# Kernel optimization log

Hardware: AMD Instinct MI355X
Metric: run time of the kernel (lower is better)

Reference implementation:

```python
import math
import jax, jax.numpy as jnp
import numpy as np

D_MODEL = 1024
NUM_HEADS = 16
HEAD_DIM = D_MODEL // NUM_HEADS
CAUSAL = True


def setup_inputs() -> dict:
    key = jax.random.key(0)
    ks = jax.random.split(key, 9)
    B, S = 2, 2048
    s = 1.0 / math.sqrt(D_MODEL)
    x = jax.random.normal(ks[0], (B, S, D_MODEL), dtype=jnp.float32)
    Wq = jax.random.normal(ks[1], (D_MODEL, D_MODEL), dtype=jnp.float32) * s
    bq = jax.random.normal(ks[2], (D_MODEL,), dtype=jnp.float32) * 0.01
    Wk = jax.random.normal(ks[3], (D_MODEL, D_MODEL), dtype=jnp.float32) * s
    bk = jax.random.normal(ks[4], (D_MODEL,), dtype=jnp.float32) * 0.01
    Wv = jax.random.normal(ks[5], (D_MODEL, D_MODEL), dtype=jnp.float32) * s
    bv = jax.random.normal(ks[6], (D_MODEL,), dtype=jnp.float32) * 0.01
    Wo = jax.random.normal(ks[7], (D_MODEL, D_MODEL), dtype=jnp.float32) * s
    bo = jax.random.normal(ks[8], (D_MODEL,), dtype=jnp.float32) * 0.01
    return {"x": x, "Wq": Wq, "bq": bq, "Wk": Wk, "bk": bk,
            "Wv": Wv, "bv": bv, "Wo": Wo, "bo": bo}


def reference(x, Wq, bq, Wk, bk, Wv, bv, Wo, bo):
    B, S, _ = x.shape
    # projections (torch Linear: x @ W.T + b; here W already stored as [in,out])
    q = x @ Wq + bq
    k = x @ Wk + bk
    v = x @ Wv + bv
    # split heads -> [B, H, S, hd]
    def split(t):
        return t.reshape(B, S, NUM_HEADS, HEAD_DIM).transpose(0, 2, 1, 3)
    q, k, v = split(q), split(k), split(v)
    scores = jnp.einsum('bhqd,bhkd->bhqk', q, k) / math.sqrt(HEAD_DIM)
    if CAUSAL:
        causal = jnp.tril(jnp.ones((S, S), dtype=bool))  # True = keep
        scores = jnp.where(causal, scores, -jnp.inf)
    attn = jax.nn.softmax(scores, axis=-1)
    out = jnp.einsum('bhqk,bhkd->bhqd', attn, v)
    out = out.transpose(0, 2, 1, 3).reshape(B, S, D_MODEL)
    return out @ Wo + bo
```

## Files before the change

### kernel.cpp

```cpp
#include <hip/hip_runtime.h>
#include <hip/hip_bf16.h>

typedef __bf16 bf16_t;
typedef __bf16 v8bf __attribute__((ext_vector_type(8)));
typedef float  v4f  __attribute__((ext_vector_type(4)));

#define MFMA16(a, b, c) __builtin_amdgcn_mfma_f32_16x16x32_bf16((a), (b), (c), 0, 0, 0)

#define GLDS16(g, l) __builtin_amdgcn_global_load_lds(                         \
    (const __attribute__((address_space(1))) void*)(g),                        \
    (__attribute__((address_space(3))) void*)(l), 16, 0, 0)

#define VMEMCNT(n) asm volatile("s_waitcnt vmcnt(" #n ")" ::: "memory")
#define SBAR()     __builtin_amdgcn_s_barrier()
#define SFENCE()   __builtin_amdgcn_sched_barrier(0)

#define B_SZ   2
#define SEQ    2048
#define DM     1024
#define NH     16
#define HD     64
#define M_TOT  4096

#define QSCALE 0.18033688011112043f

__global__ __launch_bounds__(256)
void conv_x_kernel(const float* __restrict__ src, bf16_t* __restrict__ dst)
{
    int i = (blockIdx.x * 256 + threadIdx.x) * 8;
    float4 a = *reinterpret_cast<const float4*>(src + i);
    float4 b = *reinterpret_cast<const float4*>(src + i + 4);
    union { bf16_t h[8]; int4 v; } u;
    u.h[0] = (bf16_t)a.x; u.h[1] = (bf16_t)a.y; u.h[2] = (bf16_t)a.z; u.h[3] = (bf16_t)a.w;
    u.h[4] = (bf16_t)b.x; u.h[5] = (bf16_t)b.y; u.h[6] = (bf16_t)b.z; u.h[7] = (bf16_t)b.w;
    *reinterpret_cast<int4*>(dst + i) = u.v;
}

__global__ __launch_bounds__(256)
void conv_wt_kernel(const float* __restrict__ Wq, const float* __restrict__ Wk,
                    const float* __restrict__ Wv, const float* __restrict__ Wo,
                    bf16_t* __restrict__ WqkvT, bf16_t* __restrict__ WoT)
{
    __shared__ float t[32][33];
    const int z = blockIdx.z;
    const float* src = (z == 0) ? Wq : (z == 1) ? Wk : (z == 2) ? Wv : Wo;
    bf16_t* dst = (z < 3) ? (WqkvT + (size_t)z * 1048576) : WoT;
    const int tx = threadIdx.x & 31, ty = threadIdx.x >> 5;
    const int c0 = blockIdx.x * 32, r0 = blockIdx.y * 32;
#pragma unroll
    for (int i = 0; i < 4; ++i)
        t[ty + i * 8][tx] = src[(size_t)(r0 + ty + i * 8) * DM + c0 + tx];
    __syncthreads();
#pragma unroll
    for (int i = 0; i < 4; ++i)
        dst[(size_t)(c0 + ty + i * 8) * DM + r0 + tx] = (bf16_t)t[tx][ty + i * 8];
}

__global__ __launch_bounds__(256)
void gemm_qkv_kernel(const bf16_t* __restrict__ A, const bf16_t* __restrict__ BT,
                     const float* __restrict__ b0, const float* __restrict__ b1,
                     const float* __restrict__ b2,
                     bf16_t* __restrict__ oQ, bf16_t* __restrict__ oK,
                     bf16_t* __restrict__ oV)
{
    __shared__ __align__(16) bf16_t As[2 * 128 * 64];
    __shared__ __align__(16) bf16_t Bs[2 * 192 * 64];

    const int tid  = threadIdx.x;
    const int lane = tid & 63;
    const int wave = tid >> 6;
    const int wm   = (wave >> 1) * 64;
    const int wn   = (wave & 1) * 96;
    const int quad = lane >> 4;
    const int l15  = lane & 15;
    const int l7   = l15 & 7;

    const int n0 = blockIdx.x * 192;
    const int m0 = blockIdx.y * 128;

    const bf16_t *ap[4], *bp[6];
#pragma unroll
    for (int i = 0; i < 4; ++i) {
        int cidx = (wave * 4 + i) * 64 + lane;
        int r = cidx >> 3;
        int c = (cidx & 7) ^ (r & 7);
        ap[i] = A + (size_t)(m0 + r) * DM + c * 8;
    }
#pragma unroll
    for (int i = 0; i < 6; ++i) {
        int cidx = (wave * 6 + i) * 64 + lane;
        int r = cidx >> 3;
        int c = (cidx & 7) ^ (r & 7);
        bp[i] = BT + (size_t)(n0 + r) * DM + c * 8;
    }

    const v4f vzero = {0.f, 0.f, 0.f, 0.f};
    v4f acc[4][6];
#pragma unroll
    for (int mt = 0; mt < 4; ++mt)
#pragma unroll
        for (int nt = 0; nt < 6; ++nt) acc[mt][nt] = vzero;

#pragma unroll
    for (int i = 0; i < 4; ++i) { GLDS16(ap[i], As + (wave * 4 + i) * 512); ap[i] += 64; }
#pragma unroll
    for (int i = 0; i < 6; ++i) { GLDS16(bp[i], Bs + (wave * 6 + i) * 512); bp[i] += 64; }
#pragma unroll
    for (int i = 0; i < 4; ++i) { GLDS16(ap[i], As + 8192 + (wave * 4 + i) * 512); ap[i] += 64; }
#pragma unroll
    for (int i = 0; i < 6; ++i) { GLDS16(bp[i], Bs + 12288 + (wave * 6 + i) * 512); bp[i] += 64; }

    for (int it = 0; it < 16; ++it) {
        const int cur = it & 1;
        if (it < 15) { VMEMCNT(10); } else { VMEMCNT(0); }
        SBAR(); SFENCE();
#pragma unroll
        for (int ks = 0; ks < 2; ++ks) {
            v8bf af[4], bfq[6];
#pragma unroll
            for (int mt = 0; mt < 4; ++mt)
                af[mt] = *reinterpret_cast<const v8bf*>(
                    &As[cur * 8192 + (wm + mt * 16 + l15) * 64 + ((ks * 4 + quad) ^ l7) * 8]);
#pragma unroll
            for (int nt = 0; nt < 6; ++nt)
                bfq[nt] = *reinterpret_cast<const v8bf*>(
                    &Bs[cur * 12288 + (wn + nt * 16 + l15) * 64 + ((ks * 4 + quad) ^ l7) * 8]);
#pragma unroll
            for (int mt = 0; mt < 4; ++mt)
#pragma unroll
                for (int nt = 0; nt < 6; ++nt)
                    acc[mt][nt] = MFMA16(bfq[nt], af[mt], acc[mt][nt]);
        }
        SFENCE(); SBAR();
        if (it < 14) {
#pragma unroll
            for (int i = 0; i < 4; ++i) {
                GLDS16(ap[i], As + cur * 8192 + (wave * 4 + i) * 512);
                ap[i] += 64;
            }
#pragma unroll
            for (int i = 0; i < 6; ++i) {
                GLDS16(bp[i], Bs + cur * 12288 + (wave * 6 + i) * 512);
                bp[i] += 64;
            }
        }
    }

#pragma unroll
    for (int nt = 0; nt < 6; ++nt) {
        const int cf0 = n0 + wn + nt * 16;
        const int mat = cf0 >> 10;
        const int cw  = cf0 & 1023;
        if (mat != 2) {
            bf16_t* dst = (mat == 0) ? oQ : oK;
            const float scale = (mat == 0) ? QSCALE : 1.0f;
            const float* bias = (mat == 0) ? b0 : b1;
            const int h = cw >> 6;
            const int dbase = (cw & 63) + quad * 4;
            float4 bv = *reinterpret_cast<const float4*>(bias + cw + quad * 4);
#pragma unroll
            for (int mt = 0; mt < 4; ++mt) {
                int srow = m0 + wm + mt * 16 + l15;
                int b = srow >> 11, s = srow & 2047;
                union { bf16_t hh[4]; int2 v; } u;
                u.hh[0] = (bf16_t)((acc[mt][nt][0] + bv.x) * scale);
                u.hh[1] = (bf16_t)((acc[mt][nt][1] + bv.y) * scale);
                u.hh[2] = (bf16_t)((acc[mt][nt][2] + bv.z) * scale);
                u.hh[3] = (bf16_t)((acc[mt][nt][3] + bv.w) * scale);
                *reinterpret_cast<int2*>(
                    dst + ((size_t)(b * NH + h) * SEQ + s) * HD + dbase) = u.v;
            }
        } else {
#pragma unroll
            for (int r = 0; r < 4; ++r) {
                int cwe = cw + quad * 4 + r;
                float bvv = b2[cwe];
                int h = cwe >> 6, d = cwe & 63;
#pragma unroll
                for (int mt = 0; mt < 4; ++mt) {
                    int srow = m0 + wm + mt * 16 + l15;
                    int b = srow >> 11, s = srow & 2047;
                    oV[((size_t)(b * NH + h) * HD + d) * SEQ + s] =
                        (bf16_t)(acc[mt][nt][r] + bvv);
                }
            }
        }
    }
}

__global__ __launch_bounds__(256)
void gemm_o_kernel(const bf16_t* __restrict__ A, const bf16_t* __restrict__ BT,
                   const float* __restrict__ bias, float* __restrict__ out)
{
    __shared__ __align__(16) bf16_t As[2 * 128 * 64];
    __shared__ __align__(16) bf16_t Bs[2 * 64 * 64];

    const int tid  = threadIdx.x;
    const int lane = tid & 63;
    const int wave = tid >> 6;
    const int wm   = (wave >> 1) * 64;
    const int wn   = (wave & 1) * 32;
    const int quad = lane >> 4;
    const int l15  = lane & 15;
    const int l7   = l15 & 7;

    const int n0 = blockIdx.x * 64;
    const int m0 = blockIdx.y * 128;

    const bf16_t *ap[4], *bp[2];
#pragma unroll
    for (int i = 0; i < 4; ++i) {
        int cidx = (wave * 4 + i) * 64 + lane;
        int r = cidx >> 3;
        int c = (cidx & 7) ^ (r & 7);
        ap[i] = A + (size_t)(m0 + r) * DM + c * 8;
    }
#pragma unroll
    for (int i = 0; i < 2; ++i) {
        int cidx = (wave * 2 + i) * 64 + lane;
        int r = cidx >> 3;
        int c = (cidx & 7) ^ (r & 7);
        bp[i] = BT + (size_t)(n0 + r) * DM + c * 8;
    }

    const v4f vzero = {0.f, 0.f, 0.f, 0.f};
    v4f acc[4][2];
#pragma unroll
    for (int mt = 0; mt < 4; ++mt)
#pragma unroll
        for (int nt = 0; nt < 2; ++nt) acc[mt][nt] = vzero;

#pragma unroll
    for (int i = 0; i < 4; ++i) { GLDS16(ap[i], As + (wave * 4 + i) * 512); ap[i] += 64; }
#pragma unroll
    for (int i = 0; i < 2; ++i) { GLDS16(bp[i], Bs + (wave * 2 + i) * 512); bp[i] += 64; }
#pragma unroll
    for (int i = 0; i < 4; ++i) { GLDS16(ap[i], As + 8192 + (wave * 4 + i) * 512); ap[i] += 64; }
#pragma unroll
    for (int i = 0; i < 2; ++i) { GLDS16(bp[i], Bs + 4096 + (wave * 2 + i) * 512); bp[i] += 64; }

    for (int it = 0; it < 16; ++it) {
        const int cur = it & 1;
        if (it < 15) { VMEMCNT(6); } else { VMEMCNT(0); }
        SBAR(); SFENCE();
#pragma unroll
        for (int ks = 0; ks < 2; ++ks) {
            v8bf af[4], bfq[2];
#pragma unroll
            for (int mt = 0; mt < 4; ++mt)
                af[mt] = *reinterpret_cast<const v8bf*>(
                    &As[cur * 8192 + (wm + mt * 16 + l15) * 64 + ((ks * 4 + quad) ^ l7) * 8]);
#pragma unroll
            for (int nt = 0; nt < 2; ++nt)
                bfq[nt] = *reinterpret_cast<const v8bf*>(
                    &Bs[cur * 4096 + (wn + nt * 16 + l15) * 64 + ((ks * 4 + quad) ^ l7) * 8]);
#pragma unroll
            for (int mt = 0; mt < 4; ++mt)
#pragma unroll
                for (int nt = 0; nt < 2; ++nt)
                    acc[mt][nt] = MFMA16(af[mt], bfq[nt], acc[mt][nt]);
        }
        SFENCE(); SBAR();
        if (it < 14) {
#pragma unroll
            for (int i = 0; i < 4; ++i) {
                GLDS16(ap[i], As + cur * 8192 + (wave * 4 + i) * 512);
                ap[i] += 64;
            }
#pragma unroll
            for (int i = 0; i < 2; ++i) {
                GLDS16(bp[i], Bs + cur * 4096 + (wave * 2 + i) * 512);
                bp[i] += 64;
            }
        }
    }

#pragma unroll
    for (int mt = 0; mt < 4; ++mt) {
#pragma unroll
        for (int nt = 0; nt < 2; ++nt) {
            int col = n0 + wn + nt * 16 + l15;
            float bv = bias[col];
#pragma unroll
            for (int r = 0; r < 4; ++r) {
                int row = m0 + wm + mt * 16 + quad * 4 + r;
                out[(size_t)row * DM + col] = acc[mt][nt][r] + bv;
            }
        }
    }
}

__global__ __launch_bounds__(256)
void attn_kernel(const bf16_t* __restrict__ Q, const bf16_t* __restrict__ K,
                 const bf16_t* __restrict__ Vt, bf16_t* __restrict__ O)
{
    __shared__ __align__(16) bf16_t Ks[3][64 * 64];
    __shared__ __align__(16) bf16_t Vs[3][64 * 64];
    __shared__ __align__(16) bf16_t Ps[64 * 72];

    const int tid  = threadIdx.x;
    const int lane = tid & 63;
    const int w    = tid >> 6;
    const int quad = lane >> 4;
    const int l15  = lane & 15;
    const int l7   = lane & 7;

    const int bid = blockIdx.x;
    const int xcd = bid & 7;
    const int j   = bid >> 3;
    const int bh  = (xcd << 2) | (j >> 4);
    const int p   = j & 15;
    const size_t base = (size_t)bh * SEQ * HD;
    const bf16_t* Qg = Q  + base;
    const bf16_t* Kg = K  + base;
    const bf16_t* Vg = Vt + base;

    const int rr0 = tid >> 3;
    const int cc0 = (tid & 7) ^ (rr0 & 7);
    const int bO = bh >> 4, hO = bh & 15;
    const v4f vzero = {0.f, 0.f, 0.f, 0.f};

    for (int phase = 0; phase < 2; ++phase) {
        const int t  = phase ? (31 - p) : p;
        const int q0 = t * 64;
        const int qg = q0 + w * 16 + l15;

        v8bf qf[2];
        {
            const bf16_t* qrow = Qg + (size_t)qg * HD;
            qf[0] = *reinterpret_cast<const v8bf*>(qrow + quad * 8);
            qf[1] = *reinterpret_cast<const v8bf*>(qrow + 32 + quad * 8);
        }

        const bf16_t* kp0 = Kg + (size_t)rr0 * HD + cc0 * 8;
        const bf16_t* kp1 = kp0 + 32 * HD;
        const bf16_t* vp0 = Vg + (size_t)rr0 * SEQ + cc0 * 8;
        const bf16_t* vp1 = vp0 + (size_t)32 * SEQ;

        v4f acc_o[4];
#pragma unroll
        for (int dt = 0; dt < 4; ++dt) acc_o[dt] = vzero;
        float lrow = 0.f;

        VMEMCNT(0);
        SBAR();
        GLDS16(kp0, &Ks[0][w * 512]);
        GLDS16(kp1, &Ks[0][2048 + w * 512]);
        GLDS16(vp0, &Vs[0][w * 512]);
        GLDS16(vp1, &Vs[0][2048 + w * 512]);
        kp0 += 64 * HD;  kp1 += 64 * HD;  vp0 += 64;  vp1 += 64;
        if (t >= 1) {
            GLDS16(kp0, &Ks[1][w * 512]);
            GLDS16(kp1, &Ks[1][2048 + w * 512]);
            GLDS16(vp0, &Vs[1][w * 512]);
            GLDS16(vp1, &Vs[1][2048 + w * 512]);
            kp0 += 64 * HD;  kp1 += 64 * HD;  vp0 += 64;  vp1 += 64;
        }
        if (t >= 2) {
            GLDS16(kp0, &Ks[2][w * 512]);
            GLDS16(kp1, &Ks[2][2048 + w * 512]);
            GLDS16(vp0, &Vs[2][w * 512]);
            GLDS16(vp1, &Vs[2][2048 + w * 512]);
            kp0 += 64 * HD;  kp1 += 64 * HD;  vp0 += 64;  vp1 += 64;
        }

        int cur = 0;
        for (int kt = 0; kt <= t; ++kt) {
            if (kt + 2 <= t)      { VMEMCNT(8); }
            else if (kt + 1 <= t) { VMEMCNT(4); }
            else                  { VMEMCNT(0); }
            SBAR(); SFENCE();

            v4f st[4];
#pragma unroll
            for (int ktile = 0; ktile < 4; ++ktile) st[ktile] = vzero;
#pragma unroll
            for (int ks = 0; ks < 2; ++ks) {
                v8bf kb[4];
#pragma unroll
                for (int ktile = 0; ktile < 4; ++ktile)
                    kb[ktile] = *reinterpret_cast<const v8bf*>(
                        &Ks[cur][(ktile * 16 + l15) * 64 + ((ks * 4 + quad) ^ l7) * 8]);
#pragma unroll
                for (int ktile = 0; ktile < 4; ++ktile)
                    st[ktile] = MFMA16(kb[ktile], qf[ks], st[ktile]);
            }

            const bool diagI = (kt == t);
            float rs = 0.f;
            const int prow = (w * 16 + l15) * 72;
#pragma unroll
            for (int ktile = 0; ktile < 4; ++ktile) {
                union { bf16_t h[4]; int2 v; } u;
                if (diagI && ktile > w) {
                    u.v.x = 0; u.v.y = 0;
                } else if (diagI && ktile == w) {
#pragma unroll
                    for (int r = 0; r < 4; ++r) {
                        int kg = kt * 64 + ktile * 16 + quad * 4 + r;
                        float pv = (kg > qg) ? 0.f : __builtin_amdgcn_exp2f(st[ktile][r]);
                        rs += pv;
                        u.h[r] = (bf16_t)pv;
                    }
                } else {
#pragma unroll
                    for (int r = 0; r < 4; ++r) {
                        float pv = __builtin_amdgcn_exp2f(st[ktile][r]);
                        rs += pv;
                        u.h[r] = (bf16_t)pv;
                    }
                }
                *reinterpret_cast<int2*>(&Ps[prow + ktile * 16 + quad * 4]) = u.v;
            }
            rs += __shfl_xor(rs, 16);
            rs += __shfl_xor(rs, 32);
            lrow += rs;

#pragma unroll
            for (int ks = 0; ks < 2; ++ks) {
                v8bf vb[4];
#pragma unroll
                for (int dt = 0; dt < 4; ++dt)
                    vb[dt] = *reinterpret_cast<const v8bf*>(
                        &Vs[cur][(dt * 16 + l15) * 64 + ((ks * 4 + quad) ^ l7) * 8]);
                v8bf pf = *reinterpret_cast<const v8bf*>(
                    &Ps[(w * 16 + l15) * 72 + ks * 32 + quad * 8]);
#pragma unroll
                for (int dt = 0; dt < 4; ++dt)
                    acc_o[dt] = MFMA16(vb[dt], pf, acc_o[dt]);
            }

            SFENCE(); SBAR();
            if (kt + 3 <= t) {
                GLDS16(kp0, &Ks[cur][w * 512]);
                GLDS16(kp1, &Ks[cur][2048 + w * 512]);
                GLDS16(vp0, &Vs[cur][w * 512]);
                GLDS16(vp1, &Vs[cur][2048 + w * 512]);
                kp0 += 64 * HD;  kp1 += 64 * HD;  vp0 += 64;  vp1 += 64;
            }
            cur = (cur == 2) ? 0 : cur + 1;
        }

        float rinv = 1.f / lrow;
        int s = q0 + w * 16 + l15;
#pragma unroll
        for (int dt = 0; dt < 4; ++dt) {
            union { bf16_t h[4]; int2 v; } u;
#pragma unroll
            for (int r = 0; r < 4; ++r)
                u.h[r] = (bf16_t)(acc_o[dt][r] * rinv);
            *reinterpret_cast<int2*>(
                &O[((size_t)bO * SEQ + s) * DM + hO * 64 + dt * 16 + quad * 4]) = u.v;
        }
    }
}

extern "C" void kernel_launch(void* const* d_in, const int* in_sizes, int n_in,
                              void* d_out, int out_size, void* d_ws, size_t ws_size,
                              hipStream_t stream) {
    const float* x  = (const float*)d_in[0];
    const float* Wq = (const float*)d_in[1];
    const float* bq = (const float*)d_in[2];
    const float* Wk = (const float*)d_in[3];
    const float* bk = (const float*)d_in[4];
    const float* Wv = (const float*)d_in[5];
    const float* bv = (const float*)d_in[6];
    const float* Wo = (const float*)d_in[7];
    const float* bo = (const float*)d_in[8];

    bf16_t* ws = (bf16_t*)d_ws;
    bf16_t* xb     = ws;
    bf16_t* WqkvT  = ws + 4194304;
    bf16_t* WoT    = ws + 7340032;
    bf16_t* Qb     = ws + 8388608;
    bf16_t* Kb     = ws + 12582912;
    bf16_t* Vb     = ws + 16777216;
    bf16_t* Ob     = ws;

    conv_x_kernel<<<2048, 256, 0, stream>>>(x, xb);
    conv_wt_kernel<<<dim3(32, 32, 4), 256, 0, stream>>>(Wq, Wk, Wv, Wo, WqkvT, WoT);
    gemm_qkv_kernel<<<dim3(16, 32), 256, 0, stream>>>(xb, WqkvT, bq, bk, bv, Qb, Kb, Vb);
    attn_kernel<<<512, 256, 0, stream>>>(Qb, Kb, Vb, Ob);
    gemm_o_kernel<<<dim3(16, 32), 256, 0, stream>>>(Ob, WoT, bo, (float*)d_out);
}
```

Baseline: 178.3 us.

## Split attention key tiles across waves and reduce partial outputs in LDS

Changes the attention kernel so each wave takes a 16-key slice of every key tile for all 64 queries, rather than 16 queries over all keys. The softmax probabilities now stay in registers and feed the PV MFMA directly, which removes the P round trip through shared memory and the per-tile row-sum shuffles. The cost is half-empty PV MFMAs, because only 16 of the 32 k-slots are filled and the rest are zero-padded. It also adds an end-of-phase cross-wave reduction of the output accumulators and row sums through LDS, with extra barriers.

New measurement: 179.1 us. No clear change (+0.4%).

```diff
diff --git a/kernel.cpp b/kernel.cpp
--- a/kernel.cpp
+++ b/kernel.cpp
@@ -296,7 +296,8 @@
 {
     __shared__ __align__(16) bf16_t Ks[3][64 * 64];
     __shared__ __align__(16) bf16_t Vs[3][64 * 64];
-    __shared__ __align__(16) bf16_t Ps[64 * 72];
+    __shared__ float Ored[4 * 1040];
+    __shared__ float lred[4 * 64];
 
     const int tid  = threadIdx.x;
     const int lane = tid & 63;
@@ -323,13 +324,13 @@
     for (int phase = 0; phase < 2; ++phase) {
         const int t  = phase ? (31 - p) : p;
         const int q0 = t * 64;
-        const int qg = q0 + w * 16 + l15;
-
-        v8bf qf[2];
-        {
-            const bf16_t* qrow = Qg + (size_t)qg * HD;
-            qf[0] = *reinterpret_cast<const v8bf*>(qrow + quad * 8);
-            qf[1] = *reinterpret_cast<const v8bf*>(qrow + 32 + quad * 8);
+
+        v8bf qf[4][2];
+#pragma unroll
+        for (int g = 0; g < 4; ++g) {
+            const bf16_t* qrow = Qg + (size_t)(q0 + g * 16 + l15) * HD;
+            qf[g][0] = *reinterpret_cast<const v8bf*>(qrow + quad * 8);
+            qf[g][1] = *reinterpret_cast<const v8bf*>(qrow + 32 + quad * 8);
         }
 
         const bf16_t* kp0 = Kg + (size_t)rr0 * HD + cc0 * 8;
@@ -337,10 +338,12 @@
         const bf16_t* vp0 = Vg + (size_t)rr0 * SEQ + cc0 * 8;
         const bf16_t* vp1 = vp0 + (size_t)32 * SEQ;
 
-        v4f acc_o[4];
-#pragma unroll
-        for (int dt = 0; dt < 4; ++dt) acc_o[dt] = vzero;
-        float lrow = 0.f;
+        v4f acc_p[4][4];
+#pragma unroll
+        for (int dt = 0; dt < 4; ++dt)
+#pragma unroll
+            for (int g = 0; g < 4; ++g) acc_p[dt][g] = vzero;
+        float lp[4] = {0.f, 0.f, 0.f, 0.f};
 
         VMEMCNT(0);
         SBAR();
@@ -373,61 +376,56 @@
 
             v4f st[4];
 #pragma unroll
-            for (int ktile = 0; ktile < 4; ++ktile) st[ktile] = vzero;
+            for (int g = 0; g < 4; ++g) st[g] = vzero;
 #pragma unroll
             for (int ks = 0; ks < 2; ++ks) {
-                v8bf kb[4];
-#pragma unroll
-                for (int ktile = 0; ktile < 4; ++ktile)
-                    kb[ktile] = *reinterpret_cast<const v8bf*>(
-                        &Ks[cur][(ktile * 16 + l15) * 64 + ((ks * 4 + quad) ^ l7) * 8]);
-#pragma unroll
-                for (int ktile = 0; ktile < 4; ++ktile)
-                    st[ktile] = MFMA16(kb[ktile], qf[ks], st[ktile]);
+                v8bf kf = *reinterpret_cast<const v8bf*>(
+                    &Ks[cur][(16 * w + l15) * 64 + ((ks * 4 + quad) ^ l7) * 8]);
+#pragma unroll
+                for (int g = 0; g < 4; ++g)
+                    st[g] = MFMA16(kf, qf[g][ks], st[g]);
             }
 
             const bool diagI = (kt == t);
-            float rs = 0.f;
-            const int prow = (w * 16 + l15) * 72;
-#pragma unroll
-            for (int ktile = 0; ktile < 4; ++ktile) {
-                union { bf16_t h[4]; int2 v; } u;
-                if (diagI && ktile > w) {
-                    u.v.x = 0; u.v.y = 0;
-                } else if (diagI && ktile == w) {
+            v8bf pa[4];
+#pragma unroll
+            for (int g = 0; g < 4; ++g) {
+                union { bf16_t h[8]; v8bf v; } up;
+                up.h[4] = (bf16_t)0.f; up.h[5] = (bf16_t)0.f;
+                up.h[6] = (bf16_t)0.f; up.h[7] = (bf16_t)0.f;
+                if (diagI && g < w) {
+                    up.h[0] = (bf16_t)0.f; up.h[1] = (bf16_t)0.f;
+                    up.h[2] = (bf16_t)0.f; up.h[3] = (bf16_t)0.f;
+                } else if (diagI && g == w) {
 #pragma unroll
                     for (int r = 0; r < 4; ++r) {
-                        int kg = kt * 64 + ktile * 16 + quad * 4 + r;
-                        float pv = (kg > qg) ? 0.f : __builtin_amdgcn_exp2f(st[ktile][r]);
-                        rs += pv;
-                        u.h[r] = (bf16_t)pv;
+                        float pv = (quad * 4 + r > l15)
+                                     ? 0.f : __builtin_amdgcn_exp2f(st[g][r]);
+                        lp[g] += pv;
+                        up.h[r] = (bf16_t)pv;
                     }
                 } else {
 #pragma unroll
                     for (int r = 0; r < 4; ++r) {
-                        float pv = __builtin_amdgcn_exp2f(st[ktile][r]);
-                        rs += pv;
-                        u.h[r] = (bf16_t)pv;
+                        float pv = __builtin_amdgcn_exp2f(st[g][r]);
+                        lp[g] += pv;
+                        up.h[r] = (bf16_t)pv;
                     }
                 }
-                *reinterpret_cast<int2*>(&Ps[prow + ktile * 16 + quad * 4]) = u.v;
-            }
-            rs += __shfl_xor(rs, 16);
-            rs += __shfl_xor(rs, 32);
-            lrow += rs;
-
-#pragma unroll
-            for (int ks = 0; ks < 2; ++ks) {
-                v8bf vb[4];
-#pragma unroll
-                for (int dt = 0; dt < 4; ++dt)
-                    vb[dt] = *reinterpret_cast<const v8bf*>(
-                        &Vs[cur][(dt * 16 + l15) * 64 + ((ks * 4 + quad) ^ l7) * 8]);
-                v8bf pf = *reinterpret_cast<const v8bf*>(
-                    &Ps[(w * 16 + l15) * 72 + ks * 32 + quad * 8]);
-#pragma unroll
-                for (int dt = 0; dt < 4; ++dt)
-                    acc_o[dt] = MFMA16(vb[dt], pf, acc_o[dt]);
+                pa[g] = up.v;
+            }
+
+#pragma unroll
+            for (int dt = 0; dt < 4; ++dt) {
+                const int rowd = dt * 16 + l15;
+                uint2 vv = *reinterpret_cast<const uint2*>(
+                    &Vs[cur][rowd * 64 +
+                             (((2 * w + (quad >> 1)) ^ l7) * 8 + (quad & 1) * 4)]);
+                union { unsigned u[4]; v8bf v; } uv;
+                uv.u[0] = vv.x; uv.u[1] = vv.y; uv.u[2] = 0u; uv.u[3] = 0u;
+#pragma unroll
+                for (int g = 0; g < 4; ++g)
+                    acc_p[dt][g] = MFMA16(uv.v, pa[g], acc_p[dt][g]);
             }
 
             SFENCE(); SBAR();
@@ -441,16 +439,44 @@
             cur = (cur == 2) ? 0 : cur + 1;
         }
 
-        float rinv = 1.f / lrow;
-        int s = q0 + w * 16 + l15;
+#pragma unroll
+        for (int g = 0; g < 4; ++g) {
+            lp[g] += __shfl_xor(lp[g], 16);
+            lp[g] += __shfl_xor(lp[g], 32);
+        }
+        if (quad == 0) {
+#pragma unroll
+            for (int g = 0; g < 4; ++g)
+                lred[w * 64 + g * 16 + l15] = lp[g];
+        }
+
+        const int qq = tid >> 2;
+        const int db = (tid & 3) * 4;
+        float linv = 0.f;
 #pragma unroll
         for (int dt = 0; dt < 4; ++dt) {
+#pragma unroll
+            for (int g = 0; g < 4; ++g)
+#pragma unroll
+                for (int r = 0; r < 4; ++r)
+                    Ored[w * 1040 + (quad * 4 + r) * 65 + g * 16 + l15] =
+                        acc_p[dt][g][r];
+            SBAR();
+            if (dt == 0)
+                linv = 1.f / (lred[qq] + lred[64 + qq] +
+                              lred[128 + qq] + lred[192 + qq]);
             union { bf16_t h[4]; int2 v; } u;
 #pragma unroll
-            for (int r = 0; r < 4; ++r)
-                u.h[r] = (bf16_t)(acc_o[dt][r] * rinv);
+            for (int e = 0; e < 4; ++e) {
+                float s = Ored[(db + e) * 65 + qq]
+                        + Ored[1040 + (db + e) * 65 + qq]
+                        + Ored[2080 + (db + e) * 65 + qq]
+                        + Ored[3120 + (db + e) * 65 + qq];
+                u.h[e] = (bf16_t)(s * linv);
+            }
             *reinterpret_cast<int2*>(
-                &O[((size_t)bO * SEQ + s) * DM + hO * 64 + dt * 16 + quad * 4]) = u.v;
+                &O[((size_t)bO * SEQ + q0 + qq) * DM + hO * 64 + dt * 16 + db]) = u.v;
+            SBAR();
         }
     }
 }
```
